# Performance work log

Hardware: AMD Instinct MI355X
Metric: run time of the kernel (lower is better)

Reference implementation:

```python
import jax, jax.numpy as jnp
import numpy as np

B, S, D, H, DH = 4, 1024, 1024, 16, 64  # batch, seq, d_model, heads, head dim (d_Q=d_K=d_V)


def setup_inputs() -> dict:
    key = jax.random.key(0)
    ks = jax.random.split(key, 12)
    std = 0.02
    return {
        "x_Q": jax.random.normal(ks[0], (B, S, D), jnp.float32),
        "x_K": jax.random.normal(ks[1], (B, S, D), jnp.float32),
        "x_V": jax.random.normal(ks[2], (B, S, D), jnp.float32),
        "src_batch_lens": jax.random.randint(ks[3], (B,), 0, S),
        # stacked per-head projection weights: [H, d_model, head_dim]
        "Wq": jax.random.normal(ks[4], (H, D, DH), jnp.float32) * std,
        "bq": jax.random.normal(ks[5], (H, DH), jnp.float32) * std,
        "Wk": jax.random.normal(ks[6], (H, D, DH), jnp.float32) * std,
        "bk": jax.random.normal(ks[7], (H, DH), jnp.float32) * std,
        "Wv": jax.random.normal(ks[8], (H, D, DH), jnp.float32) * std,
        "bv": jax.random.normal(ks[9], (H, DH), jnp.float32) * std,
        "Wo": jax.random.normal(ks[10], (D, D), jnp.float32) * std,
        "bo": jax.random.normal(ks[11], (D,), jnp.float32) * std,
    }


def reference(x_Q, x_K, x_V, src_batch_lens, Wq, bq, Wk, bk, Wv, bv, Wo, bo):
    dq = Wq.shape[-1]
    seq = x_Q.shape[1]
    # all heads at once instead of the per-head python loop
    Q = jnp.einsum('bsd,hde->bhse', x_Q, Wq) + bq[None, :, None, :]
    K = jnp.einsum('bsd,hde->bhse', x_K, Wk) + bk[None, :, None, :]
    V = jnp.einsum('bsd,hde->bhse', x_V, Wv) + bv[None, :, None, :]
    scores = jnp.einsum('bhse,bhte->bhst', Q, K) / jnp.sqrt(jnp.asarray(dq, x_Q.dtype))
    # original: matmul(diag(1..1,0..0), scores) zeroes query rows >= length
    rowmask = (jnp.arange(seq)[None, :] < src_batch_lens[:, None])  # [B, S]
    scores = scores * rowmask[:, None, :, None].astype(scores.dtype)
    A = jax.nn.softmax(scores, axis=-1)  # torch Softmax(dim=2) on [B,S,S] per head = key axis
    AV = jnp.einsum('bhst,bhtv->bhsv', A, V)
    out = AV.transpose(0, 2, 1, 3).reshape(x_Q.shape[0], seq, -1)  # concat heads on dim 2
    return out @ Wo + bo  # dropout p=0 -> identity
```

## Files before the change

### kernel.cpp

```cpp
#include <hip/hip_runtime.h>
#include <stdint.h>

typedef short v8s __attribute__((ext_vector_type(8)));
typedef short v4s __attribute__((ext_vector_type(4)));
typedef float v4f __attribute__((ext_vector_type(4)));

#define AS1 __attribute__((address_space(1)))
#define AS3 __attribute__((address_space(3)))

__device__ __forceinline__ void glds16(const void* g, void* l) {
  __builtin_amdgcn_global_load_lds((const AS1 void*)g, (AS3 void*)l, 16, 0, 0);
}

__device__ __forceinline__ short f2bf(float f) {
  uint32_t u = __float_as_uint(f);
  u += 0x7fffu + ((u >> 16) & 1u);
  return (short)(u >> 16);
}


__global__ __launch_bounds__(256) void cast3_f32_bf16(
    const float* __restrict__ a, const float* __restrict__ b, const float* __restrict__ c,
    short* __restrict__ oa, short* __restrict__ ob, short* __restrict__ oc, int n4) {
  const float* in = (blockIdx.z == 0) ? a : (blockIdx.z == 1) ? b : c;
  short* out      = (blockIdx.z == 0) ? oa : (blockIdx.z == 1) ? ob : oc;
  int i = blockIdx.x * 256 + threadIdx.x;
  if (i < n4) {
    float4 v = ((const float4*)in)[i];
    short4 o = { f2bf(v.x), f2bf(v.y), f2bf(v.z), f2bf(v.w) };
    ((short4*)out)[i] = o;
  }
}

__global__ __launch_bounds__(256) void transpose_w_all(
    const float* __restrict__ wq, const float* __restrict__ wk, const float* __restrict__ wv,
    const float* __restrict__ wo,
    short* __restrict__ oq, short* __restrict__ ok, short* __restrict__ ov,
    short* __restrict__ oo) {
  __shared__ float tile[64][65];
  const int z = blockIdx.z;
  const float* in;
  short* out;
  int C, R, rb, cb;
  if (z < 3) {
    const int slice = blockIdx.y;
    in  = ((z == 0) ? wq : (z == 1) ? wk : wv) + (size_t)slice * 65536;
    out = ((z == 0) ? oq : (z == 1) ? ok : ov) + (size_t)slice * 65536;
    C = 64; R = 1024; rb = blockIdx.x * 64; cb = 0;
  } else {
    in = wo; out = oo;
    C = 1024; R = 1024; rb = blockIdx.x * 64; cb = blockIdx.y * 64;
  }
  int t = threadIdx.x;
  int col = t & 63, r0 = t >> 6;
#pragma unroll
  for (int i = 0; i < 16; ++i) {
    int row = r0 + i * 4;
    tile[row][col] = in[(size_t)(rb + row) * C + cb + col];
  }
  __syncthreads();
#pragma unroll
  for (int i = 0; i < 16; ++i) {
    int orow = r0 + i * 4;
    out[(size_t)(cb + orow) * R + rb + col] = f2bf(tile[col][orow]);
  }
}

template <int MR>
__device__ __forceinline__ void gemm_core(const short* __restrict__ Ag,
                                          const short* __restrict__ Bg,
                                          short* As, short* Bs,
                                          v4f (&acc)[MR / 32][4]) {
  constexpr int MT = MR / 32;
  constexpr int ASZ = MR * 32;
  constexpr int BSZ = 128 * 32;
  const int tid  = threadIdx.x;
  const int lane = tid & 63;
  const int w    = tid >> 6;
  const int quad = lane >> 4;
  const int c15  = lane & 15;
  const int wr   = (w >> 1) * (MR / 2);
  const int wc   = (w & 1) * 64;

  const int r0 = tid >> 2;
  const int p0 = (tid & 3) ^ ((r0 & 3) ^ ((r0 >> 2) & 3));
  const short* a0 = Ag + (size_t)r0 * 1024 + p0 * 8;
  const short* a1 = a0 + 64 * 1024;
  const short* b0 = Bg + (size_t)r0 * 1024 + p0 * 8;
  const short* b1 = b0 + 64 * 1024;
  short* lA = As + tid * 8;
  short* lB = Bs + tid * 8;

  auto issue = [&](int t, int buf) {
    const int o = t * 32;
    glds16(a0 + o, lA + buf * ASZ);
    if constexpr (MR == 128) glds16(a1 + o, lA + buf * ASZ + 2048);
    glds16(b0 + o, lB + buf * BSZ);
    glds16(b1 + o, lB + buf * BSZ + 2048);
  };

  issue(0, 0);
  issue(1, 1);

  const int xs = (c15 & 3) ^ ((c15 >> 2) & 3);
  const int rdoff = ((quad ^ xs)) * 8;

  for (int kb = 0; kb < 32; ++kb) {
    if constexpr (MR == 128)
      asm volatile("s_waitcnt vmcnt(4)\n\ts_barrier" ::: "memory");
    else
      asm volatile("s_waitcnt vmcnt(3)\n\ts_barrier" ::: "memory");

    const int t2 = kb + 2;
    issue(t2 < 32 ? t2 : 31, t2 % 3);

    const short* Ab = As + (kb % 3) * ASZ;
    const short* Bb = Bs + (kb % 3) * BSZ;

    v8s a[MT], b[4];
#pragma unroll
    for (int mt = 0; mt < MT; ++mt)
      a[mt] = *(const v8s*)(Ab + (wr + mt * 16 + c15) * 32 + rdoff);
#pragma unroll
    for (int nt = 0; nt < 4; ++nt)
      b[nt] = *(const v8s*)(Bb + (wc + nt * 16 + c15) * 32 + rdoff);
#pragma unroll
    for (int mt = 0; mt < MT; ++mt)
#pragma unroll
      for (int nt = 0; nt < 4; ++nt)
        acc[mt][nt] = __builtin_amdgcn_mfma_f32_16x16x32_bf16(a[mt], b[nt], acc[mt][nt], 0, 0, 0);
  }
}

__global__ __launch_bounds__(256, 3) void proj_gemm(
    const short* __restrict__ xQ, const short* __restrict__ xK, const short* __restrict__ xV,
    const short* __restrict__ WqT, const short* __restrict__ WkT, const short* __restrict__ WvT,
    const float* __restrict__ bq, const float* __restrict__ bk, const float* __restrict__ bv,
    short* __restrict__ Qb, short* __restrict__ Kb, short* __restrict__ Vtb) {
  __shared__ short As[12288];
  __shared__ short Bs[12288];
  const int lin = blockIdx.x;
  const int z = lin >> 8;
  const int r = lin & 255;
  const int nb = ((r >> 3) & 7) * 128;
  const int mb = (((r & 7) << 2) + (r >> 6)) * 128;
  const short* A    = (z == 0) ? xQ  : (z == 1) ? xK  : xV;
  const short* Bt   = (z == 0) ? WqT : (z == 1) ? WkT : WvT;
  const float* bias = (z == 0) ? bq  : (z == 1) ? bk  : bv;
  short* outp       = (z == 0) ? Qb  : (z == 1) ? Kb  : Vtb;
  v4f acc[4][4] = {};
  gemm_core<128>(A + (size_t)mb * 1024, Bt + (size_t)nb * 1024, As, Bs, acc);

  const int lane = threadIdx.x & 63, w = threadIdx.x >> 6;
  const int quad = lane >> 4, c15 = lane & 15;
  const int wr = (w >> 1) * 64, wc = (w & 1) * 64;
  const bool vmode = (z == 2);
#pragma unroll
  for (int nt = 0; nt < 4; ++nt) {
    const int gn = nb + wc + nt * 16 + c15;
    const float bb = bias[gn];
    const int h = gn >> 6, e = gn & 63;
#pragma unroll
    for (int mt = 0; mt < 4; ++mt) {
      if (!vmode) {
#pragma unroll
        for (int rr = 0; rr < 4; ++rr) {
          const int gm = mb + wr + mt * 16 + quad * 4 + rr;
          const int bi = gm >> 10, s = gm & 1023;
          const size_t base = (size_t)(bi * 16 + h) * 65536;
          outp[base + (size_t)s * 64 + e] = f2bf(acc[mt][nt][rr] + bb);
        }
      } else {
        const int gm0 = mb + wr + mt * 16 + quad * 4;
        const int bi = gm0 >> 10, s0 = gm0 & 1023;
        const size_t base = (size_t)(bi * 16 + h) * 65536;
        short4 st = { f2bf(acc[mt][nt][0] + bb), f2bf(acc[mt][nt][1] + bb),
                      f2bf(acc[mt][nt][2] + bb), f2bf(acc[mt][nt][3] + bb) };
        *(short4*)&outp[base + (size_t)e * 1024 + s0] = st;
      }
    }
  }
}

__global__ __launch_bounds__(256, 3) void out_gemm(
    const short* __restrict__ AV, const short* __restrict__ WoT,
    const float* __restrict__ bo, float* __restrict__ outp) {
  __shared__ short As[6144];
  __shared__ short Bs[12288];
  const int lin = blockIdx.x;
  const int nb = ((lin >> 3) & 7) * 128;
  const int mb = (((lin & 7) << 3) + (lin >> 6)) * 64;
  v4f acc[2][4] = {};
  gemm_core<64>(AV + (size_t)mb * 1024, WoT + (size_t)nb * 1024, As, Bs, acc);
  const int lane = threadIdx.x & 63, w = threadIdx.x >> 6;
  const int quad = lane >> 4, c15 = lane & 15;
  const int wr = (w >> 1) * 32, wc = (w & 1) * 64;
#pragma unroll
  for (int nt = 0; nt < 4; ++nt) {
    const int gn = nb + wc + nt * 16 + c15;
    const float bb = bo[gn];
#pragma unroll
    for (int mt = 0; mt < 2; ++mt)
#pragma unroll
      for (int r = 0; r < 4; ++r) {
        const int gm = mb + wr + mt * 16 + quad * 4 + r;
        outp[(size_t)gm * 1024 + gn] = acc[mt][nt][r] + bb;
      }
  }
}

__global__ __launch_bounds__(512, 4) void attn_kernel(
    const short* __restrict__ Qb, const short* __restrict__ Kb,
    const short* __restrict__ Vtb, const int* __restrict__ lens,
    short* __restrict__ AVb) {
  __shared__ short Ks[2][4096];
  __shared__ short Vs[2][4096];
  const int tid = threadIdx.x, lane = tid & 63, w = tid >> 6;
  const int quad = lane >> 4, c15 = lane & 15;
  const int flat = blockIdx.x;
  const int bh = (flat & 7) + 8 * ((flat >> 3) & 7);
  const int qg = flat >> 6;
  const int b = bh >> 4, h = bh & 15;
  const short* Qp = Qb  + (size_t)bh * 65536;
  const short* Kp = Kb  + (size_t)bh * 65536;
  const short* Vp = Vtb + (size_t)bh * 65536;
  const int len = lens[b];
  const int row0 = qg * 128 + w * 16;

  v8s bq_[2];
#pragma unroll
  for (int kf = 0; kf < 2; ++kf)
    bq_[kf] = *(const v8s*)(Qp + (size_t)(row0 + c15) * 64 + kf * 32 + quad * 8);

  const float scale = (row0 + c15 < len) ? 0.125f : 0.0f;
  float sm = 0.f;
  v4f o[4] = {};

  const int srow = tid >> 3, spart = tid & 7;
  const int gpart = spart ^ (srow & 7);
  const int kgo = srow * 64 + gpart * 8;
  const int vgo = srow * 1024 + gpart * 8;
  const int l0 = tid * 8;

  const int c7 = c15 & 7;
  const int krow = c15 * 128;
  const int koff0 = krow + ((quad) ^ c7) * 16;
  const int koff1 = krow + ((4 + quad) ^ c7) * 16;
  const int q2 = quad >> 1, h8 = (quad & 1) * 8;
  int voff[4];
#pragma unroll
  for (int nt = 0; nt < 4; ++nt)
    voff[nt] = krow + ((2 * nt + q2) ^ c7) * 16 + h8;

  glds16(Kp + kgo, (char*)Ks[0] + l0 * 2);
  glds16(Vp + vgo, (char*)Vs[0] + l0 * 2);

  for (int kb = 0; kb < 16; ++kb) {
    const int cur = kb & 1, nxt = cur ^ 1;
    __syncthreads();

    if (kb < 15) {
      glds16(Kp + (size_t)(kb + 1) * 4096 + kgo, (char*)Ks[nxt] + l0 * 2);
      glds16(Vp + (kb + 1) * 64 + vgo, (char*)Vs[nxt] + l0 * 2);
    }

    v8s ak[4][2];
#pragma unroll
    for (int nt = 0; nt < 4; ++nt) {
      ak[nt][0] = *(const v8s*)((const char*)Ks[cur] + nt * 2048 + koff0);
      ak[nt][1] = *(const v8s*)((const char*)Ks[cur] + nt * 2048 + koff1);
    }

    v4f sc[4];
#pragma unroll
    for (int nt = 0; nt < 4; ++nt) {
      v4f z = {};
#pragma unroll
      for (int kf = 0; kf < 2; ++kf)
        z = __builtin_amdgcn_mfma_f32_16x16x32_bf16(ak[nt][kf], bq_[kf], z, 0, 0, 0);
      sc[nt] = z;
    }

    v4s pb[4];
#pragma unroll
    for (int nt = 0; nt < 4; ++nt) {
      v4s pv;
#pragma unroll
      for (int r = 0; r < 4; ++r) {
        float p = __expf(sc[nt][r] * scale);
        sm += p;
        pv[r] = f2bf(p);
      }
      pb[nt] = pv;
    }

    v4s av[4][4];
#pragma unroll
    for (int t = 0; t < 4; ++t)
#pragma unroll
      for (int nt = 0; nt < 4; ++nt)
        av[t][nt] = *(const v4s*)((const char*)Vs[cur] + t * 2048 + voff[nt]);

#pragma unroll
    for (int t = 0; t < 4; ++t)
#pragma unroll
      for (int nt = 0; nt < 4; ++nt)
        o[t] = __builtin_amdgcn_mfma_f32_16x16x16bf16_1k(av[t][nt], pb[nt], o[t], 0, 0, 0);
  }

  sm += __shfl_xor(sm, 16);
  sm += __shfl_xor(sm, 32);

  const float inv = 1.0f / sm;
  const size_t rowbase = (size_t)(b * 1024 + row0 + c15) * 1024 + h * 64;
#pragma unroll
  for (int t = 0; t < 4; ++t) {
    short4 st = { f2bf(o[t][0] * inv), f2bf(o[t][1] * inv),
                  f2bf(o[t][2] * inv), f2bf(o[t][3] * inv) };
    *(short4*)&AVb[rowbase + t * 16 + quad * 4] = st;
  }
}

extern "C" void kernel_launch(void* const* d_in, const int* in_sizes, int n_in,
                              void* d_out, int out_size, void* d_ws, size_t ws_size,
                              hipStream_t stream) {
  const float* xQ = (const float*)d_in[0];
  const float* xK = (const float*)d_in[1];
  const float* xV = (const float*)d_in[2];
  const int* lens = (const int*)d_in[3];
  const float* Wq = (const float*)d_in[4];
  const float* bq = (const float*)d_in[5];
  const float* Wk = (const float*)d_in[6];
  const float* bk = (const float*)d_in[7];
  const float* Wv = (const float*)d_in[8];
  const float* bv = (const float*)d_in[9];
  const float* Wo = (const float*)d_in[10];
  const float* bo = (const float*)d_in[11];
  float* out = (float*)d_out;

  char* ws = (char*)d_ws;
  short* xQb = (short*)(ws + 0);
  short* xKb = (short*)(ws + 8388608);
  short* xVb = (short*)(ws + 16777216);
  short* WqT = (short*)(ws + 25165824);
  short* WkT = (short*)(ws + 27262976);
  short* WvT = (short*)(ws + 29360128);
  short* WoT = (short*)(ws + 31457280);
  short* Qb  = (short*)(ws + 33554432);
  short* Kb  = (short*)(ws + 41943040);
  short* Vtb = (short*)(ws + 50331648);
  short* AVb = (short*)(ws + 58720256);

  cast3_f32_bf16<<<dim3(4096, 1, 3), 256, 0, stream>>>(xQ, xK, xV, xQb, xKb, xVb, 1048576);
  transpose_w_all<<<dim3(16, 16, 4), 256, 0, stream>>>(Wq, Wk, Wv, Wo, WqT, WkT, WvT, WoT);
  proj_gemm<<<dim3(768), 256, 0, stream>>>(xQb, xKb, xVb, WqT, WkT, WvT,
                                           bq, bk, bv, Qb, Kb, Vtb);
  attn_kernel<<<dim3(512), 512, 0, stream>>>(Qb, Kb, Vtb, lens, AVb);
  out_gemm<<<dim3(512), 256, 0, stream>>>(AVb, WoT, bo, out);
}
```

Baseline: 205.2 us.

## Merge cast and weight-transpose launches; halve attention block to 4 waves

Merges the input cast kernel and the weight transpose kernel into one prep kernel that dispatches on a flat block index, which saves one launch. The attention kernel now runs 256-thread blocks that each cover 64 query rows instead of 128. The grid doubles to 1024 blocks, and each thread issues two async K/V tile loads per stage to fill LDS. This gives more blocks for better CU occupancy and balance, at the cost of loading each K/V tile twice as often per query row.

```diff
diff --git a/kernel.cpp b/kernel.cpp
--- a/kernel.cpp
+++ b/kernel.cpp
@@ -18,41 +18,42 @@
   return (short)(u >> 16);
 }
 
-
-__global__ __launch_bounds__(256) void cast3_f32_bf16(
-    const float* __restrict__ a, const float* __restrict__ b, const float* __restrict__ c,
-    short* __restrict__ oa, short* __restrict__ ob, short* __restrict__ oc, int n4) {
-  const float* in = (blockIdx.z == 0) ? a : (blockIdx.z == 1) ? b : c;
-  short* out      = (blockIdx.z == 0) ? oa : (blockIdx.z == 1) ? ob : oc;
-  int i = blockIdx.x * 256 + threadIdx.x;
-  if (i < n4) {
+__global__ __launch_bounds__(256) void prep_kernel(
+    const float* __restrict__ xQ, const float* __restrict__ xK, const float* __restrict__ xV,
+    const float* __restrict__ wq, const float* __restrict__ wk, const float* __restrict__ wv,
+    const float* __restrict__ wo,
+    short* __restrict__ oxQ, short* __restrict__ oxK, short* __restrict__ oxV,
+    short* __restrict__ oq, short* __restrict__ ok, short* __restrict__ ov,
+    short* __restrict__ oo) {
+  const int bid = blockIdx.x;
+  const int t = threadIdx.x;
+  if (bid >= 1024) {
+    const int c = bid - 1024;
+    const int z = c >> 12;
+    const int i = (c & 4095) * 256 + t;
+    const float* in = (z == 0) ? xQ : (z == 1) ? xK : xV;
+    short* out      = (z == 0) ? oxQ : (z == 1) ? oxK : oxV;
     float4 v = ((const float4*)in)[i];
     short4 o = { f2bf(v.x), f2bf(v.y), f2bf(v.z), f2bf(v.w) };
     ((short4*)out)[i] = o;
-  }
-}
-
-__global__ __launch_bounds__(256) void transpose_w_all(
-    const float* __restrict__ wq, const float* __restrict__ wk, const float* __restrict__ wv,
-    const float* __restrict__ wo,
-    short* __restrict__ oq, short* __restrict__ ok, short* __restrict__ ov,
-    short* __restrict__ oo) {
+    return;
+  }
   __shared__ float tile[64][65];
-  const int z = blockIdx.z;
   const float* in;
   short* out;
   int C, R, rb, cb;
-  if (z < 3) {
-    const int slice = blockIdx.y;
-    in  = ((z == 0) ? wq : (z == 1) ? wk : wv) + (size_t)slice * 65536;
-    out = ((z == 0) ? oq : (z == 1) ? ok : ov) + (size_t)slice * 65536;
-    C = 64; R = 1024; rb = blockIdx.x * 64; cb = 0;
+  if (bid < 768) {
+    const int which = bid >> 8, rem = bid & 255;
+    const int slice = rem >> 4, rbi = rem & 15;
+    in  = ((which == 0) ? wq : (which == 1) ? wk : wv) + (size_t)slice * 65536;
+    out = ((which == 0) ? oq : (which == 1) ? ok : ov) + (size_t)slice * 65536;
+    C = 64; R = 1024; rb = rbi * 64; cb = 0;
   } else {
+    const int r = bid - 768;
     in = wo; out = oo;
-    C = 1024; R = 1024; rb = blockIdx.x * 64; cb = blockIdx.y * 64;
-  }
-  int t = threadIdx.x;
-  int col = t & 63, r0 = t >> 6;
+    C = 1024; R = 1024; rb = (r >> 4) * 64; cb = (r & 15) * 64;
+  }
+  const int col = t & 63, r0 = t >> 6;
 #pragma unroll
   for (int i = 0; i < 16; ++i) {
     int row = r0 + i * 4;
@@ -209,7 +210,7 @@
   }
 }
 
-__global__ __launch_bounds__(512, 4) void attn_kernel(
+__global__ __launch_bounds__(256, 4) void attn_kernel(
     const short* __restrict__ Qb, const short* __restrict__ Kb,
     const short* __restrict__ Vtb, const int* __restrict__ lens,
     short* __restrict__ AVb) {
@@ -225,7 +226,7 @@
   const short* Kp = Kb  + (size_t)bh * 65536;
   const short* Vp = Vtb + (size_t)bh * 65536;
   const int len = lens[b];
-  const int row0 = qg * 128 + w * 16;
+  const int row0 = qg * 64 + w * 16;
 
   v8s bq_[2];
 #pragma unroll
@@ -238,9 +239,9 @@
 
   const int srow = tid >> 3, spart = tid & 7;
   const int gpart = spart ^ (srow & 7);
-  const int kgo = srow * 64 + gpart * 8;
-  const int vgo = srow * 1024 + gpart * 8;
-  const int l0 = tid * 8;
+  const int kgo0 = srow * 64 + gpart * 8, kgo1 = (srow + 32) * 64 + gpart * 8;
+  const int vgo0 = srow * 1024 + gpart * 8, vgo1 = (srow + 32) * 1024 + gpart * 8;
+  const int l0 = tid * 8, l1 = 2048 + tid * 8;
 
   const int c7 = c15 & 7;
   const int krow = c15 * 128;
@@ -252,16 +253,22 @@
   for (int nt = 0; nt < 4; ++nt)
     voff[nt] = krow + ((2 * nt + q2) ^ c7) * 16 + h8;
 
-  glds16(Kp + kgo, (char*)Ks[0] + l0 * 2);
-  glds16(Vp + vgo, (char*)Vs[0] + l0 * 2);
+  glds16(Kp + kgo0, (char*)Ks[0] + l0 * 2);
+  glds16(Kp + kgo1, (char*)Ks[0] + l1 * 2);
+  glds16(Vp + vgo0, (char*)Vs[0] + l0 * 2);
+  glds16(Vp + vgo1, (char*)Vs[0] + l1 * 2);
 
   for (int kb = 0; kb < 16; ++kb) {
     const int cur = kb & 1, nxt = cur ^ 1;
     __syncthreads();
 
     if (kb < 15) {
-      glds16(Kp + (size_t)(kb + 1) * 4096 + kgo, (char*)Ks[nxt] + l0 * 2);
-      glds16(Vp + (kb + 1) * 64 + vgo, (char*)Vs[nxt] + l0 * 2);
+      const short* kt = Kp + (size_t)(kb + 1) * 4096;
+      const short* vt = Vp + (kb + 1) * 64;
+      glds16(kt + kgo0, (char*)Ks[nxt] + l0 * 2);
+      glds16(kt + kgo1, (char*)Ks[nxt] + l1 * 2);
+      glds16(vt + vgo0, (char*)Vs[nxt] + l0 * 2);
+      glds16(vt + vgo1, (char*)Vs[nxt] + l1 * 2);
     }
 
     v8s ak[4][2];
@@ -351,10 +358,10 @@
   short* Vtb = (short*)(ws + 50331648);
   short* AVb = (short*)(ws + 58720256);
 
-  cast3_f32_bf16<<<dim3(4096, 1, 3), 256, 0, stream>>>(xQ, xK, xV, xQb, xKb, xVb, 1048576);
-  transpose_w_all<<<dim3(16, 16, 4), 256, 0, stream>>>(Wq, Wk, Wv, Wo, WqT, WkT, WvT, WoT);
+  prep_kernel<<<dim3(13312), 256, 0, stream>>>(xQ, xK, xV, Wq, Wk, Wv, Wo,
+                                               xQb, xKb, xVb, WqT, WkT, WvT, WoT);
   proj_gemm<<<dim3(768), 256, 0, stream>>>(xQb, xKb, xVb, WqT, WkT, WvT,
                                            bq, bk, bv, Qb, Kb, Vtb);
-  attn_kernel<<<dim3(512), 512, 0, stream>>>(Qb, Kb, Vtb, lens, AVb);
+  attn_kernel<<<dim3(1024), 256, 0, stream>>>(Qb, Kb, Vtb, lens, AVb);
   out_gemm<<<dim3(512), 256, 0, stream>>>(AVb, WoT, bo, out);
 }
```

After: 203.1 us. No clear change (-1.1%).
